# Kernel optimization log

Measured on AMD Instinct MI355X. Metric: run time of the kernel, lower is better.

## Reference

```python
import jax, jax.numpy as jnp
import numpy as np
import math

D_MODEL = 1024
RPN_D = 256
SUP_HW = 20  # support feature map is 20x20 -> 400 tokens


def _positional_encoding(max_len, d_model):
    pos = np.arange(max_len, dtype=np.float32)[:, None]
    div = np.exp(np.arange(0, d_model, 2, dtype=np.float32) * -(math.log(10000.0) / float(d_model)))
    pe = np.zeros((max_len, d_model), dtype=np.float32)
    pe[:, 0::2] = np.sin(pos * div)
    pe[:, 1::2] = np.cos(pos * div)
    return jnp.asarray(pe)


def setup_inputs() -> dict:
    key = jax.random.key(0)
    ks = jax.random.split(key, 6)
    B, S, H = 4, 5, 4
    fh, fw = 64, 64
    base_feat = jax.random.normal(ks[0], (B, D_MODEL, fh, fw), dtype=jnp.float32)
    support_feat = jax.random.normal(ks[1], (B, S, D_MODEL, SUP_HW, SUP_HW), dtype=jnp.float32)
    Qw = jax.random.normal(ks[2], (H, RPN_D, D_MODEL), dtype=jnp.float32) * 0.01
    Qb = jnp.zeros((H, RPN_D), dtype=jnp.float32)
    Kw = jax.random.normal(ks[3], (H, RPN_D, D_MODEL), dtype=jnp.float32) * 0.01
    Kb = jnp.zeros((H, RPN_D), dtype=jnp.float32)
    Mw = jax.random.normal(ks[4], (D_MODEL, H * D_MODEL), dtype=jnp.float32) * 0.02
    Mb = jnp.zeros((D_MODEL,), dtype=jnp.float32)
    return {"base_feat": base_feat, "support_feat": support_feat,
            "Qw": Qw, "Qb": Qb, "Kw": Kw, "Kb": Kb, "Mw": Mw, "Mb": Mb}


def reference(base_feat, support_feat, Qw, Qb, Kw, Kb, Mw, Mb):
    B, C, fh, fw = base_feat.shape
    S = support_feat.shape[1]
    H = Qw.shape[0]
    Lq = fh * fw
    Lk = SUP_HW * SUP_HW

    # support_mat: [S, B, Lk, C]  (transpose(0,1) then flatten spatial, then transpose)
    support_mat = jnp.transpose(support_feat, (1, 0, 2, 3, 4)).reshape(S, B, C, Lk)
    support_mat = jnp.transpose(support_mat, (0, 1, 3, 2))
    # query_mat: [B, Lq, C]
    query_mat = jnp.transpose(base_feat.reshape(B, C, Lq), (0, 2, 1))

    pe = _positional_encoding(400, D_MODEL)[:Lk]  # [Lk, C]
    s_mat = support_mat + pe[None, None]          # [S, B, Lk, C]

    # per-head projections (q is independent of shot, compute once)
    q = jnp.einsum('blc,hdc->hbld', query_mat, Qw) + Qb[:, None, None, :]   # [H,B,Lq,d]
    k = jnp.einsum('sbkc,hdc->hsbkd', s_mat, Kw) + Kb[:, None, None, None, :]  # [H,S,B,Lk,d]

    scores = jnp.einsum('hbld,hsbkd->hsblk', q, k) / math.sqrt(RPN_D)  # [H,S,B,Lq,Lk]
    attn = jax.nn.softmax(scores, axis=-1)
    z = jnp.einsum('hsblk,sbkc->hsblc', attn, s_mat)  # [H,S,B,Lq,C]

    # shot_mode == 'mean'
    z = jnp.mean(z, axis=1)  # [H,B,Lq,C]

    # concat heads along feature dim (head order preserved): [B,Lq,H*C]
    att = jnp.transpose(z, (1, 2, 0, 3)).reshape(B, Lq, H * C)
    att = jax.nn.relu(att @ Mw.T + Mb)  # [B,Lq,C]

    att = jnp.transpose(att, (0, 2, 1)).reshape(B, C, fh, fw)
    # attention_type == 'product'
    correlation_feat = base_feat * att
    return correlation_feat
```

## Files before the change

kernel.cpp:

```cpp
#include <hip/hip_runtime.h>
#include <stdint.h>

#define DEVI __device__ __forceinline__

typedef __attribute__((ext_vector_type(8))) short bf16x8;
typedef __attribute__((ext_vector_type(4))) float f32x4;
typedef __attribute__((ext_vector_type(4))) unsigned short us4;
typedef unsigned short u16;

constexpr int B_ = 4, S_ = 5, H_ = 4, C_ = 1024, D_ = 256;
constexpr int LQ = 4096, LK = 400;

DEVI u16 f2b(float f){
  uint32_t x = __float_as_uint(f);
  uint32_t r = (x + 0x7FFFu + ((x >> 16) & 1u)) >> 16;
  return (u16)r;
}

typedef __attribute__((address_space(1))) const void ASG;
typedef __attribute__((address_space(3))) void ASL;
DEVI void gload16(const void* g, void* l){
  __builtin_amdgcn_global_load_lds((ASG*)g, (ASL*)l, 16, 0, 0);
}

__global__ __launch_bounds__(256) void k_cvt3(
    const float* __restrict__ s0, u16* __restrict__ d0, int n0,
    const float* __restrict__ s1, u16* __restrict__ d1, int n1,
    const float* __restrict__ s2, u16* __restrict__ d2, int n2){
  int i = blockIdx.x*256 + threadIdx.x;
  const float* s; u16* d; int idx;
  if (i < n0){ s = s0; d = d0; idx = i; }
  else if (i < n0 + n1){ s = s1; d = d1; idx = i - n0; }
  else if (i < n0 + n1 + n2){ s = s2; d = d2; idx = i - n0 - n1; }
  else return;
  float4 v = ((const float4*)s)[idx];
  us4 o; o.x = f2b(v.x); o.y = f2b(v.y); o.z = f2b(v.z); o.w = f2b(v.w);
  *(us4*)(d + (size_t)idx*4) = o;
}

__global__ __launch_bounds__(256) void k_transpose_x(const float* __restrict__ base, u16* __restrict__ Xb){
  __shared__ float t[32][33];
  int l0 = blockIdx.x*32, c0 = blockIdx.y*32, b = blockIdx.z;
  int tx = threadIdx.x & 31, ty = threadIdx.x >> 5;
  const float* src = base + ((size_t)b*C_ + c0)*LQ + l0;
  #pragma unroll
  for (int i=0;i<4;i++){ int cc = ty + i*8; t[cc][tx] = src[(size_t)cc*LQ + tx]; }
  __syncthreads();
  u16* dst = Xb + ((size_t)b*LQ + l0)*C_ + c0;
  #pragma unroll
  for (int i=0;i<4;i++){ int ll = ty + i*8; dst[(size_t)ll*C_ + tx] = f2b(t[tx][ll]); }
}

__global__ __launch_bounds__(256) void k_build_smat(const float* __restrict__ sup, u16* __restrict__ kc){
  __shared__ float t[32][33];
  int p0 = blockIdx.x*32, c0 = blockIdx.y*32;
  int s = blockIdx.z / B_, b = blockIdx.z % B_;
  int tx = threadIdx.x & 31, ty = threadIdx.x >> 5;
  const float* src = sup + ((size_t)(b*S_ + s)*C_ + c0)*LK + p0;
  #pragma unroll
  for (int i=0;i<4;i++){
    int cc = ty + i*8;
    int p = p0 + tx;
    int c = c0 + cc;
    float v = 0.f;
    if (p < LK){
      v = src[(size_t)cc*LK + tx];
      float dv = expf(-(float)(c & ~1) * (9.210340371976184f / 1024.f));
      float arg = (float)p * dv;
      v += (c & 1) ? cosf(arg) : sinf(arg);
    }
    t[cc][tx] = v;
  }
  __syncthreads();
  u16* dkc = kc + ((size_t)((b*S_ + s)*400 + p0))*C_ + c0;
  #pragma unroll
  for (int i=0;i<4;i++){
    int pp = ty + i*8;
    if (p0 + pp < 400) dkc[(size_t)pp*C_ + tx] = f2b(t[tx][pp]);
  }
}

DEVI void stage_half(const u16* P, int64_t ld, u16* dst, int wid, int r8, int s8){
  #pragma unroll
  for (int it=0; it<2; ++it){
    int ck = wid + it*8;
    gload16(P + (size_t)(ck*8 + r8)*ld + s8*8, dst + ck*512);
  }
}
DEVI bf16x8 ldsread(const u16* base, int row, int kk, int lane){
  int sl = ((kk<<2) + (lane>>4)) ^ (row & 7);
  return *(const bf16x8*)&base[row*64 + sl*8];
}

template<int CEPI, bool FIRST, bool FINAL, bool BIAS>
__global__ __launch_bounds__(512,1) void k8(
    const u16* __restrict__ A, const u16* __restrict__ Bm, void* __restrict__ Cm,
    const float* __restrict__ bias, const float* __restrict__ basep, const float* __restrict__ Mb,
    int tilesM, int64_t lda, int64_t ldb, int64_t ldc, int NT,
    int bdiv, int64_t aS0, int64_t aS1, int64_t bS0, int64_t bS1,
    int64_t cS0, int64_t cS1, int64_t aZ, int64_t bZ, int64_t cZ,
    int biasS0, float scale, int Nmax, int Mmax, int swz){
  __shared__ __align__(16) u16 lds[2][2][16384];
  int tid = threadIdx.x, lane = tid & 63, wid = tid >> 6;
  int bx = blockIdx.x;
  int mt, ntile;
  if (swz == 2){ int x = bx & 7, j = bx >> 3; mt = 2*x + (j >> 2); ntile = j & 3; }
  else {
    if (swz == 1) bx = (bx & 7) * (gridDim.x >> 3) + (bx >> 3);
    mt = bx % tilesM; ntile = bx / tilesM;
  }
  int z = blockIdx.y, i0 = z / bdiv, i1 = z % bdiv;
  int iz = blockIdx.z;
  const u16* Ab = A + i0*aS0 + i1*aS1 + iz*aZ + (size_t)mt*256*lda;
  const u16* Bb = Bm + i0*bS0 + i1*bS1 + iz*bZ + (size_t)ntile*256*ldb;
  int r8 = lane >> 3, s8 = (lane & 7) ^ r8;
  int wr = wid >> 2, wc = wid & 3;

  f32x4 acc[8][4];
  #pragma unroll
  for (int i=0;i<8;i++)
    #pragma unroll
    for (int j=0;j<4;j++) acc[i][j] = (f32x4){0.f,0.f,0.f,0.f};

  const u16 *ApS = Ab, *BpS = Bb;
  stage_half(ApS,                   lda, &lds[0][0][0],    wid, r8, s8);
  stage_half(ApS + (size_t)128*lda, lda, &lds[0][0][8192], wid, r8, s8);
  stage_half(BpS,                   ldb, &lds[0][1][0],    wid, r8, s8);
  stage_half(BpS + (size_t)128*ldb, ldb, &lds[0][1][8192], wid, r8, s8);
  ApS += 64; BpS += 64;

  for (int t = 0; t < NT; ++t){
    int cur = t & 1, nxt = cur ^ 1;
    bool pf = (t + 1 < NT);
    const u16* lA = &lds[cur][0][0];
    const u16* lB = &lds[cur][1][0];
    u16* sA = &lds[nxt][0][0];
    u16* sB = &lds[nxt][1][0];
    if (pf){
      stage_half(ApS,                   lda, sA,        wid, r8, s8);
      stage_half(ApS + (size_t)128*lda, lda, sA + 8192, wid, r8, s8);
      asm volatile("s_waitcnt vmcnt(4)" ::: "memory");
    } else {
      asm volatile("s_waitcnt vmcnt(0)" ::: "memory");
    }
    asm volatile("s_barrier" ::: "memory");

    bf16x8 bfr[4][2];
    #pragma unroll
    for (int jn=0;jn<4;jn++)
      #pragma unroll
      for (int kk=0;kk<2;kk++)
        bfr[jn][kk] = ldsread(lB, wc*64 + jn*16 + (lane & 15), kk, lane);

    #pragma unroll
    for (int p = 0; p < 4; ++p){
      bf16x8 af[2][2];
      #pragma unroll
      for (int dm=0;dm<2;dm++)
        #pragma unroll
        for (int kk=0;kk<2;kk++)
          af[dm][kk] = ldsread(lA, wr*128 + (p*2+dm)*16 + (lane & 15), kk, lane);
      __builtin_amdgcn_s_setprio(1);
      #pragma unroll
      for (int dm=0;dm<2;dm++)
        #pragma unroll
        for (int jn=0;jn<4;jn++)
          #pragma unroll
          for (int kk=0;kk<2;kk++)
            acc[p*2+dm][jn] = __builtin_amdgcn_mfma_f32_16x16x32_bf16(af[dm][kk], bfr[jn][kk], acc[p*2+dm][jn], 0,0,0);
      __builtin_amdgcn_s_setprio(0);
      if (p == 0 && pf) stage_half(BpS,                   ldb, sB,        wid, r8, s8);
      if (p == 1 && pf) stage_half(BpS + (size_t)128*ldb, ldb, sB + 8192, wid, r8, s8);
    }
    asm volatile("s_barrier" ::: "memory");
    if (pf){ ApS += 64; BpS += 64; }
  }

  int g = lane >> 4, c16 = lane & 15;
  if constexpr (CEPI == 0){
    u16* Cb = (u16*)Cm + i0*cS0 + i1*cS1 + iz*cZ;
    #pragma unroll
    for (int jn=0;jn<4;jn++){
      int n = ntile*256 + wc*64 + jn*16 + c16;
      if (n >= Nmax) continue;
      float bv = 0.f;
      if (BIAS) bv = bias[(size_t)i0*biasS0 + n];
      #pragma unroll
      for (int im=0;im<8;im++){
        int m = mt*256 + wr*128 + im*16 + g*4;
        if (m >= Mmax) continue;
        #pragma unroll
        for (int r=0;r<4;r++)
          Cb[(size_t)(m + r)*ldc + n] = f2b((acc[im][jn][r] + bv)*scale);
      }
    }
  } else {
    float* Cb = (float*)Cm + i0*cS0 + i1*cS1 + iz*cZ;
    const float* Bs = basep + i0*cS0 + i1*cS1 + iz*cZ;
    #pragma unroll
    for (int jn=0;jn<4;jn++){
      int n = ntile*256 + wc*64 + jn*16 + c16;
      float mbv = 0.f;
      if (FINAL) mbv = Mb[n];
      #pragma unroll
      for (int im=0;im<8;im++){
        int m = mt*256 + wr*128 + im*16 + g*4;
        float* p = Cb + (size_t)n*ldc + m;
        float4 v;
        v.x = acc[im][jn][0]; v.y = acc[im][jn][1]; v.z = acc[im][jn][2]; v.w = acc[im][jn][3];
        if (!FIRST){
          float4 old = *(const float4*)p;
          v.x += old.x; v.y += old.y; v.z += old.z; v.w += old.w;
        }
        if (FINAL){
          float4 bs = *(const float4*)(Bs + (size_t)n*ldc + m);
          v.x = bs.x * fmaxf(0.2f*v.x + mbv, 0.f);
          v.y = bs.y * fmaxf(0.2f*v.y + mbv, 0.f);
          v.z = bs.z * fmaxf(0.2f*v.z + mbv, 0.f);
          v.w = bs.w * fmaxf(0.2f*v.w + mbv, 0.f);
        }
        *(float4*)p = v;
      }
    }
  }
}

__global__ __launch_bounds__(512) void k_scores(
    const u16* __restrict__ qws, const u16* __restrict__ kws,
    u16* __restrict__ attn, int h0, int KVP, int padw, int nz){
  __shared__ __align__(16) u16 lQ[128*64];
  __shared__ __align__(16) u16 lK[400*64];
  int tid = threadIdx.x, lane = tid & 63, wid = tid >> 6;
  int m0 = blockIdx.x * 128;
  int b = blockIdx.y;
  int zz = blockIdx.z;
  int s = zz % 5, h = h0 + zz / 5;
  const u16* Qp = qws + ((size_t)(h*B_ + b)*LQ + m0)*D_;
  const u16* Kp = kws + ((size_t)((h*B_ + b)*2000 + s*400))*D_;
  int r8 = lane >> 3, s8 = (lane & 7) ^ r8;
  f32x4 acc[25];
  #pragma unroll
  for (int t=0;t<25;t++) acc[t] = (f32x4){0.f,0.f,0.f,0.f};
  int wm = wid * 16;
  for (int k0 = 0; k0 < 256; k0 += 64){
    __syncthreads();
    #pragma unroll
    for (int c = 0; c < 2; ++c){
      int cc = wid + c*8;
      int row = cc*8 + r8;
      gload16(Qp + (size_t)row*D_ + k0 + s8*8, &lQ[cc*512]);
    }
    for (int cc = wid; cc < 50; cc += 8){
      int row = cc*8 + r8;
      gload16(Kp + (size_t)row*D_ + k0 + s8*8, &lK[cc*512]);
    }
    __syncthreads();
    #pragma unroll
    for (int kk = 0; kk < 2; ++kk){
      int rowA = wm + (lane & 15);
      int slA = ((kk<<2) + (lane>>4)) ^ (rowA & 7);
      bf16x8 af = *(const bf16x8*)&lQ[rowA*64 + slA*8];
      #pragma unroll
      for (int t=0;t<25;t++){
        int rowB = t*16 + (lane & 15);
        int slB = ((kk<<2) + (lane>>4)) ^ (rowB & 7);
        bf16x8 bf = *(const bf16x8*)&lK[rowB*64 + slB*8];
        acc[t] = __builtin_amdgcn_mfma_f32_16x16x32_bf16(af, bf, acc[t], 0,0,0);
      }
    }
  }
  float mx[4] = {-1e30f,-1e30f,-1e30f,-1e30f};
  #pragma unroll
  for (int t=0;t<25;t++)
    #pragma unroll
    for (int r=0;r<4;r++) mx[r] = fmaxf(mx[r], acc[t][r]);
  #pragma unroll
  for (int r=0;r<4;r++){
    mx[r] = fmaxf(mx[r], __shfl_xor(mx[r], 1));
    mx[r] = fmaxf(mx[r], __shfl_xor(mx[r], 2));
    mx[r] = fmaxf(mx[r], __shfl_xor(mx[r], 4));
    mx[r] = fmaxf(mx[r], __shfl_xor(mx[r], 8));
  }
  float sm[4] = {0.f,0.f,0.f,0.f};
  #pragma unroll
  for (int t=0;t<25;t++)
    #pragma unroll
    for (int r=0;r<4;r++){ float e = __expf(acc[t][r] - mx[r]); acc[t][r] = e; sm[r] += e; }
  #pragma unroll
  for (int r=0;r<4;r++){
    sm[r] += __shfl_xor(sm[r], 1);
    sm[r] += __shfl_xor(sm[r], 2);
    sm[r] += __shfl_xor(sm[r], 4);
    sm[r] += __shfl_xor(sm[r], 8);
    sm[r] = 1.f / sm[r];
  }
  u16* ap = attn + ((size_t)b*LQ + m0 + wm)*KVP + (size_t)zz*400;
  int g = lane >> 4, c16 = lane & 15;
  #pragma unroll
  for (int t=0;t<25;t++)
    #pragma unroll
    for (int r=0;r<4;r++)
      ap[(size_t)(g*4 + r)*KVP + t*16 + c16] = f2b(acc[t][r] * sm[r]);
  if (zz == nz - 1 && padw > 0){
    u16* base2 = attn + ((size_t)b*LQ + m0)*KVP + (KVP - padw);
    int total = 128 * padw;
    for (int i = tid; i < total; i += 512){
      int rr = i / padw, cc = i % padw;
      base2[(size_t)rr*KVP + cc] = 0;
    }
  }
}

extern "C" void kernel_launch(void* const* d_in, const int* in_sizes, int n_in,
                              void* d_out, int out_size, void* d_ws, size_t ws_size,
                              hipStream_t stream){
  const float* base = (const float*)d_in[0];
  const float* sup  = (const float*)d_in[1];
  const float* Qw   = (const float*)d_in[2];
  const float* Qb   = (const float*)d_in[3];
  const float* Kw   = (const float*)d_in[4];
  const float* Kb   = (const float*)d_in[5];
  const float* Mw   = (const float*)d_in[6];
  const float* Mb   = (const float*)d_in[7];
  float* out = (float*)d_out;
  char* ws = (char*)d_ws;

  const int GH = (ws_size >= 247988224ull) ? 2 : 1;
  const int NG = H_ / GH;
  const int NZ = GH * 5;
  const int KVP = (NZ*400 + 63) & ~63;
  const int NT = KVP / 64;
  const int PADW = KVP - NZ*400;

  u16* wQw = (u16*)(ws + 0);
  u16* wKw = (u16*)(ws + 2097152);
  u16* wMw = (u16*)(ws + 4194304);
  u16* wKC = (u16*)(ws + 12582912);
  u16* wK  = (u16*)(ws + 30932992);
  u16* wQ  = (u16*)(ws + 49283072);
  u16* wVt = (u16*)(ws + 82837504);
  u16* wAT = (u16*)(ws + 82837504 + (size_t)B_*C_*KVP*2);
  u16* wXb = wAT;

  const int BIG = 1 << 30;

  k_cvt3<<<6144, 256, 0, stream>>>(Qw, wQw, 262144, Kw, wKw, 262144, Mw, wMw, 1048576);
  k_transpose_x<<<dim3(128, 32, 4), 256, 0, stream>>>(base, wXb);
  k_build_smat<<<dim3(13, 32, 20), 256, 0, stream>>>(sup, wKC);

  k8<0,false,false,true><<<dim3(8, 16, 1), 512, 0, stream>>>(
      wKC, wKw, wK, Kb, nullptr, nullptr,
      8, C_, C_, D_, 16,
      4, 0, (int64_t)S_*400*C_, (int64_t)D_*C_, 0,
      (int64_t)B_*2000*D_, (int64_t)2000*D_, 0, 0, 0,
      D_, 1.f, BIG, 2000, 0);

  k8<0,false,false,true><<<dim3(16, 16, 1), 512, 0, stream>>>(
      wXb, wQw, wQ, Qb, nullptr, nullptr,
      16, C_, C_, D_, 16,
      4, 0, (int64_t)LQ*C_, (int64_t)D_*C_, 0,
      (int64_t)B_*LQ*D_, (int64_t)LQ*D_, 0, 0, 0,
      D_, 1.f/16.f, BIG, BIG, 1);

  for (int g = 0; g < NG; ++g){
    k8<0,false,false,false><<<dim3(32, GH, 4), 512, 0, stream>>>(
        wMw + (size_t)(g*GH)*C_, wKC, wVt, nullptr, nullptr, nullptr,
        4, (int64_t)H_*C_, C_, KVP, 16,
        1, (int64_t)C_, 0, 0, 0,
        2000, 0, 0, (int64_t)S_*400*C_, (int64_t)C_*KVP,
        0, 1.f, 2000, BIG, 0);

    k_scores<<<dim3(32, 4, NZ), 512, 0, stream>>>(wQ, wK, wAT, g*GH, KVP, PADW, NZ);

    if (g == 0 && NG > 1){
      k8<1,true,false,false><<<dim3(64, 4, 1), 512, 0, stream>>>(
          wAT, wVt, out, nullptr, base, Mb,
          16, KVP, KVP, LQ, NT,
          1, (int64_t)LQ*KVP, 0, (int64_t)C_*KVP, 0,
          (int64_t)C_*LQ, 0, 0, 0, 0,
          0, 1.f, BIG, BIG, 2);
    } else if (g == NG - 1){
      k8<1,false,true,false><<<dim3(64, 4, 1), 512, 0, stream>>>(
          wAT, wVt, out, nullptr, base, Mb,
          16, KVP, KVP, LQ, NT,
          1, (int64_t)LQ*KVP, 0, (int64_t)C_*KVP, 0,
          (int64_t)C_*LQ, 0, 0, 0, 0,
          0, 1.f, BIG, BIG, 2);
    } else {
      k8<1,false,false,false><<<dim3(64, 4, 1), 512, 0, stream>>>(
          wAT, wVt, out, nullptr, base, Mb,
          16, KVP, KVP, LQ, NT,
          1, (int64_t)LQ*KVP, 0, (int64_t)C_*KVP, 0,
          (int64_t)C_*LQ, 0, 0, 0, 0,
          0, 1.f, BIG, BIG, 2);
    }
  }
}
```

Baseline: 661.2 us.

## Double-buffer Q/K LDS tiles in k_scores to overlap loads with MFMA

The k_scores kernel now keeps two LDS buffers for the Q and K tiles. It prefetches the next 64-wide slice of the head dimension while MFMAs run on the current slice, and replaces the per-iteration __syncthreads with explicit vmcnt waits and barriers. K loads are unrolled to a fixed 7 chunks per wave, so 448 rows are loaded instead of 400. That over-reads past the 400 real rows, and possibly past the end of the buffer for the last shot. Together with the larger LDS footprint and the __launch_bounds__(512,1) hint, this limits residency to one block per CU in exchange for hiding global-load latency.

```diff
diff --git a/kernel.cpp b/kernel.cpp
--- a/kernel.cpp
+++ b/kernel.cpp
@@ -225,11 +225,11 @@
   }
 }
 
-__global__ __launch_bounds__(512) void k_scores(
+__global__ __launch_bounds__(512,1) void k_scores(
     const u16* __restrict__ qws, const u16* __restrict__ kws,
     u16* __restrict__ attn, int h0, int KVP, int padw, int nz){
-  __shared__ __align__(16) u16 lQ[128*64];
-  __shared__ __align__(16) u16 lK[400*64];
+  __shared__ __align__(16) u16 lQ[2][128*64];
+  __shared__ __align__(16) u16 lK[2][448*64];
   int tid = threadIdx.x, lane = tid & 63, wid = tid >> 6;
   int m0 = blockIdx.x * 128;
   int b = blockIdx.y;
@@ -242,33 +242,55 @@
   #pragma unroll
   for (int t=0;t<25;t++) acc[t] = (f32x4){0.f,0.f,0.f,0.f};
   int wm = wid * 16;
-  for (int k0 = 0; k0 < 256; k0 += 64){
-    __syncthreads();
-    #pragma unroll
-    for (int c = 0; c < 2; ++c){
-      int cc = wid + c*8;
-      int row = cc*8 + r8;
-      gload16(Qp + (size_t)row*D_ + k0 + s8*8, &lQ[cc*512]);
-    }
-    for (int cc = wid; cc < 50; cc += 8){
-      int row = cc*8 + r8;
-      gload16(Kp + (size_t)row*D_ + k0 + s8*8, &lK[cc*512]);
-    }
-    __syncthreads();
+
+  #pragma unroll
+  for (int c = 0; c < 2; ++c){
+    int cc = wid + c*8;
+    gload16(Qp + (size_t)(cc*8 + r8)*D_ + s8*8, &lQ[0][cc*512]);
+  }
+  #pragma unroll
+  for (int i = 0; i < 7; ++i){
+    int ck = wid + i*8;
+    gload16(Kp + (size_t)(ck*8 + r8)*D_ + s8*8, &lK[0][ck*512]);
+  }
+
+  for (int t = 0; t < 4; ++t){
+    if (t < 3){
+      int k1 = (t+1)*64;
+      int nb = (t+1) & 1;
+      #pragma unroll
+      for (int c = 0; c < 2; ++c){
+        int cc = wid + c*8;
+        gload16(Qp + (size_t)(cc*8 + r8)*D_ + k1 + s8*8, &lQ[nb][cc*512]);
+      }
+      #pragma unroll
+      for (int i = 0; i < 7; ++i){
+        int ck = wid + i*8;
+        gload16(Kp + (size_t)(ck*8 + r8)*D_ + k1 + s8*8, &lK[nb][ck*512]);
+      }
+      asm volatile("s_waitcnt vmcnt(9)" ::: "memory");
+    } else {
+      asm volatile("s_waitcnt vmcnt(0)" ::: "memory");
+    }
+    asm volatile("s_barrier" ::: "memory");
+    const u16* lq = &lQ[t & 1][0];
+    const u16* lk = &lK[t & 1][0];
     #pragma unroll
     for (int kk = 0; kk < 2; ++kk){
       int rowA = wm + (lane & 15);
       int slA = ((kk<<2) + (lane>>4)) ^ (rowA & 7);
-      bf16x8 af = *(const bf16x8*)&lQ[rowA*64 + slA*8];
-      #pragma unroll
-      for (int t=0;t<25;t++){
-        int rowB = t*16 + (lane & 15);
+      bf16x8 af = *(const bf16x8*)&lq[rowA*64 + slA*8];
+      #pragma unroll
+      for (int tt=0;tt<25;tt++){
+        int rowB = tt*16 + (lane & 15);
         int slB = ((kk<<2) + (lane>>4)) ^ (rowB & 7);
-        bf16x8 bf = *(const bf16x8*)&lK[rowB*64 + slB*8];
-        acc[t] = __builtin_amdgcn_mfma_f32_16x16x32_bf16(af, bf, acc[t], 0,0,0);
+        bf16x8 bf = *(const bf16x8*)&lk[rowB*64 + slB*8];
+        acc[tt] = __builtin_amdgcn_mfma_f32_16x16x32_bf16(af, bf, acc[tt], 0,0,0);
       }
     }
-  }
+    asm volatile("s_barrier" ::: "memory");
+  }
+
   float mx[4] = {-1e30f,-1e30f,-1e30f,-1e30f};
   #pragma unroll
   for (int t=0;t<25;t++)
```

After: 640.2 us (median of 2 runs). -3.2%, faster.
